# Optimization experiments

Measured on AMD Instinct MI355X. Metric: run time of the kernel, lower is better.

Reference implementation:

```python
import jax, jax.numpy as jnp
import numpy as np

N, D, P, NS = 2048, 64, 32, 512  # nnodes, stop_embedding_size, preference_dim, n_active_stops
LEAKY_SLOPE = 0.01
COS_EPS = 1e-8


def setup_inputs() -> dict:
    key = jax.random.key(0)
    ks = jax.random.split(key, 10)
    dist = jax.random.uniform(ks[0], (N, N), dtype=jnp.float32)
    stops = jax.random.randint(ks[1], (NS,), 0, N)
    emb_w = jax.random.normal(ks[2], (N, D), dtype=jnp.float32) * 0.05      # nn.Embedding weight
    lin_l_w = jax.random.normal(ks[3], (P, D), dtype=jnp.float32) * 0.05    # SAGEConv lin_l (aggregated)
    lin_l_b = jnp.zeros((P,), dtype=jnp.float32)
    lin_r_w = jax.random.normal(ks[4], (P, D), dtype=jnp.float32) * 0.05    # SAGEConv lin_r (root)
    edge_w = jax.random.normal(ks[5], (2 * P,), dtype=jnp.float32) * 0.05   # edge_summarizer weight
    edge_b = jnp.zeros((), dtype=jnp.float32)
    in_len = 2 * N + 3 + P
    comb_w = jax.random.normal(ks[6], (N, in_len), dtype=jnp.float32) * 0.02  # combiner weight
    comb_b = jnp.zeros((N,), dtype=jnp.float32)
    return {
        "dist": dist, "emb_w": emb_w,
        "lin_l_w": lin_l_w, "lin_l_b": lin_l_b, "lin_r_w": lin_r_w,
        "edge_w": edge_w, "edge_b": edge_b,
        "comb_w": comb_w, "comb_b": comb_b,
        "stops": stops, "weekday": 3, "vehicles": 5,
    }


def reference(dist, emb_w, lin_l_w, lin_l_b, lin_r_w, edge_w, edge_b,
              comb_w, comb_b, stops, weekday, vehicles):
    dt = emb_w.dtype
    # --- cosine-similarity graph build ---
    norm = jnp.maximum(jnp.linalg.norm(emb_w, axis=1, keepdims=True), COS_EPS)
    xn = emb_w / norm
    sim = xn @ xn.T                                   # [N, N]
    sim = sim * (1.0 - jnp.eye(N, dtype=dt))          # fill_diagonal_(0)
    keep = jnp.zeros((N,), dtype=bool).at[stops].set(True)
    adj = ((sim > 0.5) & keep[:, None] & keep[None, :]).astype(dt)  # [N, N]
    # --- SAGEConv (mean aggregation): lin_l(mean_j x_j) + lin_r(x_i) ---
    deg = jnp.maximum(adj.sum(axis=1, keepdims=True), 1.0)
    agg = (adj @ emb_w) / deg                         # [N, D]
    pref = agg @ lin_l_w.T + lin_l_b + emb_w @ lin_r_w.T   # [N, P]
    # --- all-pairs edge summaries: Linear([pref_i, pref_j]) + LeakyReLU ---
    # equivalent to concat-then-linear, without materializing [N^2, 2P]
    a = pref @ edge_w[:P]                             # [N]
    b = pref @ edge_w[P:]                             # [N]
    es = a[:, None] + b[None, :] + edge_b             # [N, N]
    es = jnp.where(es >= 0, es, LEAKY_SLOPE * es)
    # --- combiner + log-softmax ---
    weekday_feat = jnp.full((N, 1), weekday, dtype=dt)
    vehicle_feat = jnp.full((N, 1), vehicles, dtype=dt)
    stop_feat = keep.astype(dt)[:, None]
    combined = jnp.concatenate([pref, es, dist, weekday_feat, vehicle_feat, stop_feat], axis=1)
    out = combined @ comb_w.T + comb_b                # [N, N]
    return jax.nn.log_softmax(out, axis=1)
```

## Files before the change

### kernel.cpp

```cpp
#include <hip/hip_runtime.h>

typedef unsigned short u16;
typedef __attribute__((ext_vector_type(8))) short bf16x8;
typedef __attribute__((ext_vector_type(4))) float f32x4;

__device__ __forceinline__ u16 f2bf(float f) {
    return (u16)((__float_as_uint(f) + 0x8000u) >> 16);
}

#define N_NODES 2048
#define D_EMB 64
#define P_DIM 32
#define NS_STOPS 512
#define IN_LEN 4131
#define NKT 65

#define SWZ(row, c) ((((row) * 8) + ((c) ^ ((row) & 7))) * 8)

__device__ __forceinline__ void gload16(const u16* g, u16* l) {
    __builtin_amdgcn_global_load_lds((const __attribute__((address_space(1))) void*)g,
                                     (__attribute__((address_space(3))) void*)l, 16, 0, 0);
}

__global__ __launch_bounds__(256) void k_aggpref(const float* __restrict__ emb, const int* __restrict__ stops,
                                                 const float* __restrict__ lin_l_w, const float* __restrict__ lin_l_b,
                                                 const float* __restrict__ lin_r_w, const float* __restrict__ edge_w,
                                                 float* __restrict__ pref, float* __restrict__ av, float* __restrict__ bv) {
    int i = blockIdx.x, t = threadIdx.x;
    __shared__ int bm[64];
    __shared__ int kl[NS_STOPS];
    __shared__ int cnt, degL;
    __shared__ float xi[D_EMB];
    __shared__ float aggL[D_EMB];
    __shared__ float niS;
    if (t < 64) bm[t] = 0;
    if (t == 0) { cnt = 0; degL = 0; }
    if (t < D_EMB) { xi[t] = emb[i * D_EMB + t]; aggL[t] = 0.f; }
    __syncthreads();
    {
        int s0 = stops[t], s1 = stops[t + 256];
        atomicOr(&bm[s0 >> 5], 1 << (s0 & 31));
        atomicOr(&bm[s1 >> 5], 1 << (s1 & 31));
    }
    __syncthreads();
    {
        int w = bm[t >> 2];
        int base = (t >> 2) * 32 + (t & 3) * 8;
        #pragma unroll
        for (int e = 0; e < 8; ++e)
            if ((w >> ((t & 3) * 8 + e)) & 1) { int p = atomicAdd(&cnt, 1); kl[p] = base + e; }
    }
    if (t < 64) {
        float s = xi[t] * xi[t];
        #pragma unroll
        for (int off = 32; off; off >>= 1) s += __shfl_xor(s, off, 64);
        if (t == 0) niS = fmaxf(sqrtf(s), 1e-8f);
    }
    __syncthreads();
    int ki = (bm[i >> 5] >> (i & 31)) & 1;
    if (ki) {
        int nk = cnt;
        float ni = niS;
        const f32x4* xiv = (const f32x4*)xi;
        for (int u = t; u < nk; u += 256) {
            int j = kl[u];
            if (j == i) continue;
            const f32x4* ej = (const f32x4*)&emb[j * D_EMB];
            f32x4 er[16];
            f32x4 dv = {0.f, 0.f, 0.f, 0.f};
            f32x4 sv = {0.f, 0.f, 0.f, 0.f};
            #pragma unroll
            for (int d = 0; d < 16; ++d) {
                er[d] = ej[d];
                dv += xiv[d] * er[d];
                sv += er[d] * er[d];
            }
            float dot = dv[0] + dv[1] + dv[2] + dv[3];
            float nj = fmaxf(sqrtf(sv[0] + sv[1] + sv[2] + sv[3]), 1e-8f);
            if (dot > 0.5f * ni * nj) {
                atomicAdd(&degL, 1);
                #pragma unroll
                for (int d = 0; d < 16; ++d) {
                    atomicAdd(&aggL[d * 4 + 0], er[d][0]);
                    atomicAdd(&aggL[d * 4 + 1], er[d][1]);
                    atomicAdd(&aggL[d * 4 + 2], er[d][2]);
                    atomicAdd(&aggL[d * 4 + 3], er[d][3]);
                }
            }
        }
    }
    __syncthreads();
    if (t < D_EMB) {
        float deg = fmaxf((float)degL, 1.0f);
        aggL[t] = ki ? (aggL[t] / deg) : 0.f;
    }
    __syncthreads();
    if (t < P_DIM) {
        float s = lin_l_b[t];
        const float* wl = &lin_l_w[t * D_EMB];
        const float* wr = &lin_r_w[t * D_EMB];
        #pragma unroll
        for (int d = 0; d < D_EMB; ++d) s += aggL[d] * wl[d] + xi[d] * wr[d];
        pref[i * P_DIM + t] = s;
        float a = s * edge_w[t];
        float b = s * edge_w[P_DIM + t];
        #pragma unroll
        for (int off = 16; off; off >>= 1) { a += __shfl_xor(a, off, 64); b += __shfl_xor(b, off, 64); }
        if (t == 0) { av[i] = a; bv[i] = b; }
    }
}

__global__ __launch_bounds__(256) void k_pack(const float* __restrict__ comb_w, const float* __restrict__ comb_b,
                                              const int* __restrict__ wk_p, const int* __restrict__ vh_p,
                                              const float* __restrict__ dist, const float* __restrict__ pref,
                                              const float* __restrict__ av, const float* __restrict__ bv,
                                              const float* __restrict__ edge_b,
                                              u16* __restrict__ Bp, u16* __restrict__ Ap,
                                              float* __restrict__ cvec, float* __restrict__ w3) {
    int kt = blockIdx.x;
    int ty = blockIdx.y;
    int t = threadIdx.x;
    if (ty < 16) {
        int nt = ty;
        u16* tb = Bp + ((size_t)nt * NKT + kt) * 8192;
        #pragma unroll
        for (int it = 0; it < 4; ++it) {
            int q = t + it * 256;
            int r = q >> 3, c = q & 7;
            int j = nt * 128 + r;
            int k0 = kt * 64 + c * 8;
            const float* cw = comb_w + (size_t)j * IN_LEN;
            bf16x8 v;
            if (k0 < 4096) {
                f32x4 f0, f1;
                __builtin_memcpy(&f0, cw + 32 + k0, 16);
                __builtin_memcpy(&f1, cw + 36 + k0, 16);
                #pragma unroll
                for (int e = 0; e < 4; ++e) { v[e] = (short)f2bf(f0[e]); v[4 + e] = (short)f2bf(f1[e]); }
            } else if (k0 < 4128) {
                f32x4 f0, f1;
                __builtin_memcpy(&f0, cw + (k0 - 4096), 16);
                __builtin_memcpy(&f1, cw + (k0 - 4092), 16);
                #pragma unroll
                for (int e = 0; e < 4; ++e) { v[e] = (short)f2bf(f0[e]); v[4 + e] = (short)f2bf(f1[e]); }
            } else {
                #pragma unroll
                for (int e = 0; e < 8; ++e) v[e] = 0;
            }
            *(bf16x8*)&tb[r * 64 + ((c ^ (r & 7)) * 8)] = v;
        }
        if (kt == 64 && t < 128) {
            int j = nt * 128 + t;
            const float* cw = comb_w + (size_t)j * IN_LEN;
            float wk = (float)wk_p[0], vh = (float)vh_p[0];
            cvec[j] = wk * cw[4128] + vh * cw[4129] + comb_b[j];
            w3[j] = cw[4130];
        }
    } else {
        int rt = ty - 16;
        u16* ta = Ap + ((size_t)rt * NKT + kt) * 4096;
        float eb = edge_b[0];
        #pragma unroll
        for (int it = 0; it < 2; ++it) {
            int q = t + it * 256;
            int r = q >> 3, c = q & 7;
            int row = rt * 64 + r;
            int k0 = kt * 64 + c * 8;
            bf16x8 v;
            if (k0 < 2048) {
                float ab = av[row] + eb;
                f32x4 f0 = *(const f32x4*)(bv + k0);
                f32x4 f1 = *(const f32x4*)(bv + k0 + 4);
                #pragma unroll
                for (int e = 0; e < 4; ++e) {
                    float s0 = ab + f0[e]; s0 = (s0 >= 0.f) ? s0 : 0.01f * s0;
                    float s1 = ab + f1[e]; s1 = (s1 >= 0.f) ? s1 : 0.01f * s1;
                    v[e] = (short)f2bf(s0); v[4 + e] = (short)f2bf(s1);
                }
            } else if (k0 < 4096) {
                const f32x4* dp = (const f32x4*)(dist + (size_t)row * 2048 + (k0 - 2048));
                f32x4 f0 = dp[0], f1 = dp[1];
                #pragma unroll
                for (int e = 0; e < 4; ++e) { v[e] = (short)f2bf(f0[e]); v[4 + e] = (short)f2bf(f1[e]); }
            } else if (k0 < 4128) {
                const f32x4* pp = (const f32x4*)(pref + (size_t)row * P_DIM + (k0 - 4096));
                f32x4 f0 = pp[0], f1 = pp[1];
                #pragma unroll
                for (int e = 0; e < 4; ++e) { v[e] = (short)f2bf(f0[e]); v[4 + e] = (short)f2bf(f1[e]); }
            } else {
                #pragma unroll
                for (int e = 0; e < 8; ++e) v[e] = 0;
            }
            *(bf16x8*)&ta[r * 64 + ((c ^ (r & 7)) * 8)] = v;
        }
    }
}

__global__ __launch_bounds__(256, 4) void k_gemm_d(const u16* __restrict__ Ap, const u16* __restrict__ Bp,
                                                   float* __restrict__ Cout) {
    __shared__ __attribute__((aligned(16))) short As[2][4096];
    __shared__ __attribute__((aligned(16))) short Bs[2][4096];
    int t = threadIdx.x;
    int b = blockIdx.x;
    int c = b & 7, u = b >> 3;
    int mt = (c & 1) * 16 + (u & 15);
    int nt = (c >> 1) * 8 + (u >> 4);
    int tileM = mt * 64, tileN = nt * 64;
    int lane = t & 63;
    int wid = t >> 6;
    int waveM = wid & 1, waveN = wid >> 1;
    int l16 = lane & 15, quad = lane >> 4;

    f32x4 acc[2][2];
    #pragma unroll
    for (int a_ = 0; a_ < 2; ++a_)
        #pragma unroll
        for (int b_ = 0; b_ < 2; ++b_) acc[a_][b_] = (f32x4){0.f, 0.f, 0.f, 0.f};

    const u16* gA = Ap + ((size_t)mt * NKT) * 4096 + t * 8;
    const u16* gB = Bp + ((size_t)(nt >> 1) * NKT) * 8192 + (nt & 1) * 4096 + t * 8;

#define ISSUE(ktv, bb) do { \
        const u16* a0 = gA + (size_t)(ktv) * 4096; \
        const u16* b0 = gB + (size_t)(ktv) * 8192; \
        u16* ad = (u16*)As[bb] + t * 8; \
        u16* bd = (u16*)Bs[bb] + t * 8; \
        gload16(a0, ad); \
        gload16(a0 + 2048, ad + 2048); \
        gload16(b0, bd); \
        gload16(b0 + 2048, bd + 2048); \
    } while (0)

    ISSUE(0, 0);

    int cur = 0;
    for (int kt = 0; kt < NKT; ++kt) {
        __syncthreads();
        if (kt + 1 < NKT) ISSUE(kt + 1, cur ^ 1);
        const short* Asc = As[cur];
        const short* Bsc = Bs[cur];
        #pragma unroll
        for (int kk = 0; kk < 64; kk += 32) {
            int cbase = kk >> 3;
            bf16x8 af[2], bfr[2];
            #pragma unroll
            for (int mi = 0; mi < 2; ++mi) {
                int row = waveM * 32 + mi * 16 + l16;
                af[mi] = *(const bf16x8*)&Asc[SWZ(row, cbase + quad)];
            }
            #pragma unroll
            for (int ni = 0; ni < 2; ++ni) {
                int row = waveN * 32 + ni * 16 + l16;
                bfr[ni] = *(const bf16x8*)&Bsc[SWZ(row, cbase + quad)];
            }
            #pragma unroll
            for (int mi = 0; mi < 2; ++mi)
                #pragma unroll
                for (int ni = 0; ni < 2; ++ni)
                    acc[mi][ni] = __builtin_amdgcn_mfma_f32_16x16x32_bf16(af[mi], bfr[ni], acc[mi][ni], 0, 0, 0);
        }
        cur ^= 1;
    }
#undef ISSUE
    #pragma unroll
    for (int mi = 0; mi < 2; ++mi)
        #pragma unroll
        for (int ni = 0; ni < 2; ++ni) {
            int row = tileM + waveM * 32 + mi * 16 + quad * 4;
            int col = tileN + waveN * 32 + ni * 16 + l16;
            float* cp = Cout + (size_t)row * N_NODES + col;
            #pragma unroll
            for (int rr = 0; rr < 4; ++rr) cp[(size_t)rr * N_NODES] = acc[mi][ni][rr];
        }
}

__global__ __launch_bounds__(256) void k_epi(const float* __restrict__ cvec, const float* __restrict__ w3,
                                             const int* __restrict__ stops, float* __restrict__ out) {
    int i = blockIdx.x, t = threadIdx.x;
    __shared__ int bm[64];
    __shared__ float redmax[4], redsum[4];
    if (t < 64) bm[t] = 0;
    __syncthreads();
    {
        int s0 = stops[t], s1 = stops[t + 256];
        atomicOr(&bm[s0 >> 5], 1 << (s0 & 31));
        atomicOr(&bm[s1 >> 5], 1 << (s1 & 31));
    }
    __syncthreads();
    float ki = (float)((bm[i >> 5] >> (i & 31)) & 1);
    f32x4* orow = (f32x4*)(out + (size_t)i * N_NODES);
    const f32x4* cv = (const f32x4*)cvec;
    const f32x4* wv = (const f32x4*)w3;
    f32x4 v0 = orow[t] + cv[t] + ki * wv[t];
    f32x4 v1 = orow[t + 256] + cv[t + 256] + ki * wv[t + 256];
    float vmax = fmaxf(fmaxf(fmaxf(v0[0], v0[1]), fmaxf(v0[2], v0[3])),
                       fmaxf(fmaxf(v1[0], v1[1]), fmaxf(v1[2], v1[3])));
    #pragma unroll
    for (int off = 32; off; off >>= 1) vmax = fmaxf(vmax, __shfl_xor(vmax, off, 64));
    if ((t & 63) == 0) redmax[t >> 6] = vmax;
    __syncthreads();
    vmax = fmaxf(fmaxf(redmax[0], redmax[1]), fmaxf(redmax[2], redmax[3]));
    float se = 0.f;
    #pragma unroll
    for (int e = 0; e < 4; ++e) se += expf(v0[e] - vmax) + expf(v1[e] - vmax);
    #pragma unroll
    for (int off = 32; off; off >>= 1) se += __shfl_xor(se, off, 64);
    if ((t & 63) == 0) redsum[t >> 6] = se;
    __syncthreads();
    se = redsum[0] + redsum[1] + redsum[2] + redsum[3];
    float lz = vmax + logf(se);
    orow[t] = v0 - lz;
    orow[t + 256] = v1 - lz;
}

extern "C" void kernel_launch(void* const* d_in, const int* in_sizes, int n_in,
                              void* d_out, int out_size, void* d_ws, size_t ws_size,
                              hipStream_t stream) {
    const float* dist    = (const float*)d_in[0];
    const float* emb     = (const float*)d_in[1];
    const float* lin_l_w = (const float*)d_in[2];
    const float* lin_l_b = (const float*)d_in[3];
    const float* lin_r_w = (const float*)d_in[4];
    const float* edge_w  = (const float*)d_in[5];
    const float* edge_b  = (const float*)d_in[6];
    const float* comb_w  = (const float*)d_in[7];
    const float* comb_b  = (const float*)d_in[8];
    const int* stops     = (const int*)d_in[9];
    const int* wk        = (const int*)d_in[10];
    const int* vh        = (const int*)d_in[11];

    char* ws = (char*)d_ws;
    float* pref  = (float*)(ws + 0);
    float* av    = (float*)(ws + 262144);
    float* bv    = (float*)(ws + 270336);
    float* cvec  = (float*)(ws + 278528);
    float* w3    = (float*)(ws + 286720);
    u16*   Ap    = (u16*)(ws + 294912);
    u16*   Bp    = (u16*)(ws + 17334272);
    float* out   = (float*)d_out;

    hipLaunchKernelGGL(k_aggpref, dim3(2048),   dim3(256), 0, stream, emb, stops,
                       lin_l_w, lin_l_b, lin_r_w, edge_w, pref, av, bv);
    hipLaunchKernelGGL(k_pack,    dim3(65, 48), dim3(256), 0, stream, comb_w, comb_b, wk, vh,
                       dist, pref, av, bv, edge_b, Bp, Ap, cvec, w3);
    hipLaunchKernelGGL(k_gemm_d,  dim3(1024),   dim3(256), 0, stream, Ap, Bp, out);
    hipLaunchKernelGGL(k_epi,     dim3(2048),   dim3(256), 0, stream, cvec, w3, stops, out);
}
```

Before: 192.4 us.

## Generate edge-summary tiles inside GEMM and batch aggregation over eight nodes

The leaky-ReLU edge-summary block of the A operand is now computed on the fly inside the GEMM's load stage from av/bv, so it is no longer packed to global memory and read back. The A workspace shrinks to the dist/pref half. The aggregation kernel now handles eight nodes per block, staging the active stop embeddings and their norms in shared memory once, which cuts redundant global loads and norm computation. The trade-offs are extra ALU work and synchronous LDS stores in the GEMM pipeline for half the K tiles, and a large shared-memory footprint in the aggregation kernel, which lowers its occupancy.

```diff
diff --git a/kernel.cpp b/kernel.cpp
--- a/kernel.cpp
+++ b/kernel.cpp
@@ -14,6 +14,7 @@
 #define NS_STOPS 512
 #define IN_LEN 4131
 #define NKT 65
+#define NKTA 33
 
 #define SWZ(row, c) ((((row) * 8) + ((c) ^ ((row) & 7))) * 8)
 
@@ -26,16 +27,23 @@
                                                  const float* __restrict__ lin_l_w, const float* __restrict__ lin_l_b,
                                                  const float* __restrict__ lin_r_w, const float* __restrict__ edge_w,
                                                  float* __restrict__ pref, float* __restrict__ av, float* __restrict__ bv) {
-    int i = blockIdx.x, t = threadIdx.x;
+    __shared__ float se[NS_STOPS][68];
     __shared__ int bm[64];
     __shared__ int kl[NS_STOPS];
-    __shared__ int cnt, degL;
-    __shared__ float xi[D_EMB];
-    __shared__ float aggL[D_EMB];
-    __shared__ float niS;
+    __shared__ float nrm[NS_STOPS];
+    __shared__ float xiS[8][D_EMB];
+    __shared__ float aggS[8][D_EMB];
+    __shared__ float niS[8];
+    __shared__ int degS[8];
+    __shared__ int kiS[8];
+    __shared__ int cnt;
+    int t = threadIdx.x;
+    int i0 = blockIdx.x * 8;
     if (t < 64) bm[t] = 0;
-    if (t == 0) { cnt = 0; degL = 0; }
-    if (t < D_EMB) { xi[t] = emb[i * D_EMB + t]; aggL[t] = 0.f; }
+    if (t == 0) cnt = 0;
+    if (t < 8) degS[t] = 0;
+    ((float*)aggS)[t] = 0.f;
+    ((float*)aggS)[t + 256] = 0.f;
     __syncthreads();
     {
         int s0 = stops[t], s1 = stops[t + 256];
@@ -50,71 +58,85 @@
         for (int e = 0; e < 8; ++e)
             if ((w >> ((t & 3) * 8 + e)) & 1) { int p = atomicAdd(&cnt, 1); kl[p] = base + e; }
     }
-    if (t < 64) {
-        float s = xi[t] * xi[t];
-        #pragma unroll
-        for (int off = 32; off; off >>= 1) s += __shfl_xor(s, off, 64);
-        if (t == 0) niS = fmaxf(sqrtf(s), 1e-8f);
-    }
-    __syncthreads();
-    int ki = (bm[i >> 5] >> (i & 31)) & 1;
-    if (ki) {
-        int nk = cnt;
-        float ni = niS;
-        const f32x4* xiv = (const f32x4*)xi;
-        for (int u = t; u < nk; u += 256) {
-            int j = kl[u];
-            if (j == i) continue;
-            const f32x4* ej = (const f32x4*)&emb[j * D_EMB];
-            f32x4 er[16];
+    if (t < 8) { int i = i0 + t; kiS[t] = (bm[i >> 5] >> (i & 31)) & 1; }
+    {
+        int n = t >> 5, d = (t & 31) * 2;
+        xiS[n][d]     = emb[(i0 + n) * D_EMB + d];
+        xiS[n][d + 1] = emb[(i0 + n) * D_EMB + d + 1];
+    }
+    __syncthreads();
+    int nk = cnt;
+    for (int u = t >> 3; u < nk; u += 32) {
+        int l8 = (t & 7) * 8;
+        f32x4 a = *(const f32x4*)&emb[kl[u] * D_EMB + l8];
+        f32x4 b = *(const f32x4*)&emb[kl[u] * D_EMB + l8 + 4];
+        *(f32x4*)&se[u][l8] = a;
+        *(f32x4*)&se[u][l8 + 4] = b;
+    }
+    if (t < 8) {
+        float s = 0.f;
+        #pragma unroll
+        for (int d = 0; d < D_EMB; ++d) s += xiS[t][d] * xiS[t][d];
+        niS[t] = fmaxf(sqrtf(s), 1e-8f);
+    }
+    __syncthreads();
+    for (int u = t; u < nk; u += 256) {
+        float s = 0.f;
+        #pragma unroll
+        for (int d = 0; d < 16; ++d) {
+            f32x4 v = *(const f32x4*)&se[u][d * 4];
+            s += v[0] * v[0] + v[1] * v[1] + v[2] * v[2] + v[3] * v[3];
+        }
+        nrm[u] = fmaxf(sqrtf(s), 1e-8f);
+    }
+    __syncthreads();
+    for (int u = t; u < nk; u += 256) {
+        int j = kl[u];
+        float nj = nrm[u];
+        f32x4 er[16];
+        #pragma unroll
+        for (int d = 0; d < 16; ++d) er[d] = *(const f32x4*)&se[u][d * 4];
+        #pragma unroll
+        for (int n = 0; n < 8; ++n) {
+            if (!kiS[n] || j == i0 + n) continue;
             f32x4 dv = {0.f, 0.f, 0.f, 0.f};
-            f32x4 sv = {0.f, 0.f, 0.f, 0.f};
-            #pragma unroll
-            for (int d = 0; d < 16; ++d) {
-                er[d] = ej[d];
-                dv += xiv[d] * er[d];
-                sv += er[d] * er[d];
-            }
+            #pragma unroll
+            for (int d = 0; d < 16; ++d) dv += (*(const f32x4*)&xiS[n][d * 4]) * er[d];
             float dot = dv[0] + dv[1] + dv[2] + dv[3];
-            float nj = fmaxf(sqrtf(sv[0] + sv[1] + sv[2] + sv[3]), 1e-8f);
-            if (dot > 0.5f * ni * nj) {
-                atomicAdd(&degL, 1);
+            if (dot > 0.5f * niS[n] * nj) {
+                atomicAdd(&degS[n], 1);
                 #pragma unroll
                 for (int d = 0; d < 16; ++d) {
-                    atomicAdd(&aggL[d * 4 + 0], er[d][0]);
-                    atomicAdd(&aggL[d * 4 + 1], er[d][1]);
-                    atomicAdd(&aggL[d * 4 + 2], er[d][2]);
-                    atomicAdd(&aggL[d * 4 + 3], er[d][3]);
+                    atomicAdd(&aggS[n][d * 4 + 0], er[d][0]);
+                    atomicAdd(&aggS[n][d * 4 + 1], er[d][1]);
+                    atomicAdd(&aggS[n][d * 4 + 2], er[d][2]);
+                    atomicAdd(&aggS[n][d * 4 + 3], er[d][3]);
                 }
             }
         }
     }
     __syncthreads();
-    if (t < D_EMB) {
-        float deg = fmaxf((float)degL, 1.0f);
-        aggL[t] = ki ? (aggL[t] / deg) : 0.f;
-    }
-    __syncthreads();
-    if (t < P_DIM) {
-        float s = lin_l_b[t];
-        const float* wl = &lin_l_w[t * D_EMB];
-        const float* wr = &lin_r_w[t * D_EMB];
-        #pragma unroll
-        for (int d = 0; d < D_EMB; ++d) s += aggL[d] * wl[d] + xi[d] * wr[d];
-        pref[i * P_DIM + t] = s;
-        float a = s * edge_w[t];
-        float b = s * edge_w[P_DIM + t];
-        #pragma unroll
-        for (int off = 16; off; off >>= 1) { a += __shfl_xor(a, off, 64); b += __shfl_xor(b, off, 64); }
-        if (t == 0) { av[i] = a; bv[i] = b; }
+    {
+        int n = t >> 5, p = t & 31;
+        int i = i0 + n;
+        float inv = kiS[n] ? (1.f / fmaxf((float)degS[n], 1.0f)) : 0.f;
+        float s = lin_l_b[p];
+        const float* wl = &lin_l_w[p * D_EMB];
+        const float* wr = &lin_r_w[p * D_EMB];
+        #pragma unroll
+        for (int d = 0; d < D_EMB; ++d) s += aggS[n][d] * inv * wl[d] + xiS[n][d] * wr[d];
+        pref[i * P_DIM + p] = s;
+        float a = s * edge_w[p];
+        float b = s * edge_w[P_DIM + p];
+        #pragma unroll
+        for (int off = 16; off; off >>= 1) { a += __shfl_xor(a, off, 32); b += __shfl_xor(b, off, 32); }
+        if (p == 0) { av[i] = a; bv[i] = b; }
     }
 }
 
 __global__ __launch_bounds__(256) void k_pack(const float* __restrict__ comb_w, const float* __restrict__ comb_b,
                                               const int* __restrict__ wk_p, const int* __restrict__ vh_p,
                                               const float* __restrict__ dist, const float* __restrict__ pref,
-                                              const float* __restrict__ av, const float* __restrict__ bv,
-                                              const float* __restrict__ edge_b,
                                               u16* __restrict__ Bp, u16* __restrict__ Ap,
                                               float* __restrict__ cvec, float* __restrict__ w3) {
     int kt = blockIdx.x;
@@ -157,9 +179,9 @@
             w3[j] = cw[4130];
         }
     } else {
+        if (kt < 32) return;
         int rt = ty - 16;
-        u16* ta = Ap + ((size_t)rt * NKT + kt) * 4096;
-        float eb = edge_b[0];
+        u16* ta = Ap + ((size_t)rt * NKTA + (kt - 32)) * 4096;
         #pragma unroll
         for (int it = 0; it < 2; ++it) {
             int q = t + it * 256;
@@ -167,17 +189,7 @@
             int row = rt * 64 + r;
             int k0 = kt * 64 + c * 8;
             bf16x8 v;
-            if (k0 < 2048) {
-                float ab = av[row] + eb;
-                f32x4 f0 = *(const f32x4*)(bv + k0);
-                f32x4 f1 = *(const f32x4*)(bv + k0 + 4);
-                #pragma unroll
-                for (int e = 0; e < 4; ++e) {
-                    float s0 = ab + f0[e]; s0 = (s0 >= 0.f) ? s0 : 0.01f * s0;
-                    float s1 = ab + f1[e]; s1 = (s1 >= 0.f) ? s1 : 0.01f * s1;
-                    v[e] = (short)f2bf(s0); v[4 + e] = (short)f2bf(s1);
-                }
-            } else if (k0 < 4096) {
+            if (k0 < 4096) {
                 const f32x4* dp = (const f32x4*)(dist + (size_t)row * 2048 + (k0 - 2048));
                 f32x4 f0 = dp[0], f1 = dp[1];
                 #pragma unroll
@@ -197,6 +209,8 @@
 }
 
 __global__ __launch_bounds__(256, 4) void k_gemm_d(const u16* __restrict__ Ap, const u16* __restrict__ Bp,
+                                                   const float* __restrict__ av, const float* __restrict__ bv,
+                                                   const float* __restrict__ edge_b,
                                                    float* __restrict__ Cout) {
     __shared__ __attribute__((aligned(16))) short As[2][4096];
     __shared__ __attribute__((aligned(16))) short Bs[2][4096];
@@ -210,6 +224,8 @@
     int wid = t >> 6;
     int waveM = wid & 1, waveN = wid >> 1;
     int l16 = lane & 15, quad = lane >> 4;
+    int r_ = t >> 2;
+    float avr = av[tileM + r_] + edge_b[0];
 
     f32x4 acc[2][2];
     #pragma unroll
@@ -217,18 +233,36 @@
         #pragma unroll
         for (int b_ = 0; b_ < 2; ++b_) acc[a_][b_] = (f32x4){0.f, 0.f, 0.f, 0.f};
 
-    const u16* gA = Ap + ((size_t)mt * NKT) * 4096 + t * 8;
     const u16* gB = Bp + ((size_t)(nt >> 1) * NKT) * 8192 + (nt & 1) * 4096 + t * 8;
+    const u16* gA = Ap + ((size_t)mt * NKTA) * 4096 + t * 8;
 
 #define ISSUE(ktv, bb) do { \
-        const u16* a0 = gA + (size_t)(ktv) * 4096; \
         const u16* b0 = gB + (size_t)(ktv) * 8192; \
-        u16* ad = (u16*)As[bb] + t * 8; \
         u16* bd = (u16*)Bs[bb] + t * 8; \
-        gload16(a0, ad); \
-        gload16(a0 + 2048, ad + 2048); \
         gload16(b0, bd); \
         gload16(b0 + 2048, bd + 2048); \
+        if ((ktv) < 32) { \
+            int k0 = (ktv) * 64; \
+            _Pragma("unroll") \
+            for (int cc = 0; cc < 2; ++cc) { \
+                int ch = (t & 3) * 2 + cc; \
+                f32x4 f0 = *(const f32x4*)&bv[k0 + ch * 8]; \
+                f32x4 f1 = *(const f32x4*)&bv[k0 + ch * 8 + 4]; \
+                bf16x8 v; \
+                _Pragma("unroll") \
+                for (int e = 0; e < 4; ++e) { \
+                    float s0 = avr + f0[e]; s0 = (s0 >= 0.f) ? s0 : 0.01f * s0; \
+                    float s1 = avr + f1[e]; s1 = (s1 >= 0.f) ? s1 : 0.01f * s1; \
+                    v[e] = (short)f2bf(s0); v[4 + e] = (short)f2bf(s1); \
+                } \
+                *(bf16x8*)&As[bb][SWZ(r_, ch)] = v; \
+            } \
+        } else { \
+            const u16* a0 = gA + (size_t)((ktv) - 32) * 4096; \
+            u16* ad = (u16*)As[bb] + t * 8; \
+            gload16(a0, ad); \
+            gload16(a0 + 2048, ad + 2048); \
+        } \
     } while (0)
 
     ISSUE(0, 0);
@@ -336,13 +370,13 @@
     float* cvec  = (float*)(ws + 278528);
     float* w3    = (float*)(ws + 286720);
     u16*   Ap    = (u16*)(ws + 294912);
-    u16*   Bp    = (u16*)(ws + 17334272);
+    u16*   Bp    = (u16*)(ws + 8945664);
     float* out   = (float*)d_out;
 
-    hipLaunchKernelGGL(k_aggpref, dim3(2048),   dim3(256), 0, stream, emb, stops,
+    hipLaunchKernelGGL(k_aggpref, dim3(256),    dim3(256), 0, stream, emb, stops,
                        lin_l_w, lin_l_b, lin_r_w, edge_w, pref, av, bv);
     hipLaunchKernelGGL(k_pack,    dim3(65, 48), dim3(256), 0, stream, comb_w, comb_b, wk, vh,
-                       dist, pref, av, bv, edge_b, Bp, Ap, cvec, w3);
-    hipLaunchKernelGGL(k_gemm_d,  dim3(1024),   dim3(256), 0, stream, Ap, Bp, out);
+                       dist, pref, Bp, Ap, cvec, w3);
+    hipLaunchKernelGGL(k_gemm_d,  dim3(1024),   dim3(256), 0, stream, Ap, Bp, av, bv, edge_b, out);
     hipLaunchKernelGGL(k_epi,     dim3(2048),   dim3(256), 0, stream, cvec, w3, stops, out);
 }
```

Result: slower. 206.1 us (+7.1%).
